# Performance work log

Hardware: AMD Instinct MI355X
Metric: run time of the kernel (lower is better)

The kernel has to match this reference:

```python
import jax, jax.numpy as jnp
from jax import lax
import numpy as np

# ---- config (mirrors cfg_post / cfg_proj) ----
CENTER_THRESHOLD = 0.1
NMS_KERNEL = 7
TOP_K = 128
STUFF_AREA = 2048
LABEL_DIVISOR = 1000
THING_LIST = jnp.array([1, 2, 3, 4, 5, 6, 7], dtype=jnp.int32)
DEPTH_MIN = 0.0
DEPTH_MAX = 6.0
VOXEL_SIZE = 0.0625
TRUNCATION = 3.0
TSDF_THRESH = 1.5  # not Matterport
NUM_CLASSES = 12
B, H, W, G = 2, 256, 256, 96


def setup_inputs() -> dict:
    key = jax.random.key(0)
    ks = jax.random.split(key, 7)
    semantic2d = jax.random.normal(ks[0], (B, NUM_CLASSES, H, W), jnp.float32)
    center2d = jax.random.uniform(ks[1], (B, 1, H, W), jnp.float32)
    offset2d = jax.random.normal(ks[2], (B, 2, H, W), jnp.float32) * 8.0
    geometry = jax.random.normal(ks[3], (B, 1, G, G, G), jnp.float32) * 2.0
    occupancy3d = jax.random.normal(ks[4], (B, 1, G, G, G), jnp.float32)
    semantic3d = jax.random.normal(ks[5], (B, NUM_CLASSES, G, G, G), jnp.float32)
    offset3d = jax.random.normal(ks[6], (B, 3, G, G, G), jnp.float32) * 4.0
    fx = 288.0
    intrinsic = jnp.tile(
        jnp.array([[fx, 0.0, W / 2.0], [0.0, fx, H / 2.0], [0.0, 0.0, 1.0]],
                  jnp.float32)[None], (B, 1, 1))
    return dict(semantic2d=semantic2d, center2d=center2d, offset2d=offset2d,
                geometry=geometry, occupancy3d=occupancy3d,
                semantic3d=semantic3d, offset3d=offset3d, intrinsic=intrinsic)


def _isin_things(x):
    return (x[..., None] == THING_LIST).any(-1)


def _panoptic2d(sem_logits, heat, offset):
    # sem_logits [C,H,W], heat [1,H,W], offset [2,H,W] (dy,dx)
    sem = jnp.argmax(sem_logits, axis=0).astype(jnp.int32)  # [H,W]
    hm = heat[0]
    # heatmap NMS: keep local maxima under a NMS_KERNEL max-pool
    pooled = lax.reduce_window(hm, -jnp.inf, lax.max,
                               (NMS_KERNEL, NMS_KERNEL), (1, 1), 'SAME')
    hm_nms = jnp.where(pooled == hm, hm, 0.0)
    scores, idx = lax.top_k(hm_nms.reshape(-1), TOP_K)
    valid = scores > CENTER_THRESHOLD                       # [K]
    cy = (idx // W).astype(jnp.float32)
    cx = (idx % W).astype(jnp.float32)
    classes = sem[idx // W, idx % W]                        # class at center px
    # per-pixel nearest-center assignment via predicted offsets
    yy, xx = jnp.meshgrid(jnp.arange(H, dtype=jnp.float32),
                          jnp.arange(W, dtype=jnp.float32), indexing='ij')
    py = (yy + offset[0]).reshape(-1, 1)                    # [HW,1]
    px = (xx + offset[1]).reshape(-1, 1)
    d2 = (py - cy[None, :]) ** 2 + (px - cx[None, :]) ** 2  # [HW,K]
    d2 = jnp.where(valid[None, :], d2, jnp.inf)
    inst = jnp.argmin(d2, axis=1).astype(jnp.int32)         # [HW]
    any_valid = valid.any()
    thing_mask = _isin_things(sem)
    # stuff-area filtering
    counts = jax.ops.segment_sum(jnp.ones(H * W, jnp.float32),
                                 sem.reshape(-1), num_segments=NUM_CLASSES)
    stuff_keep = counts[sem] >= STUFF_AREA
    stuff_pan = jnp.where(stuff_keep, sem * LABEL_DIVISOR, 0)
    inst2d = inst.reshape(H, W)
    thing_pan = classes[inst2d] * LABEL_DIVISOR + inst2d + 1
    thing_pan = jnp.where(any_valid, thing_pan, 0)
    pan = jnp.where(thing_mask, thing_pan, stuff_pan)
    return pan, cy, cx, scores, classes, valid


def _panoptic3d(fg, sem3d, offset3d, cy, cx, classes, valid, intr):
    # fg [G,G,G] bool, sem3d [G,G,G] int, offset3d [3,G,G,G]
    fx, fy = intr[0, 0], intr[1, 1]
    u0, v0 = intr[0, 2], intr[1, 2]
    ii, jj, kk = jnp.meshgrid(jnp.arange(G, dtype=jnp.float32),
                              jnp.arange(G, dtype=jnp.float32),
                              jnp.arange(G, dtype=jnp.float32), indexing='ij')
    # shift voxel index by 3D center offset, convert to metric camera coords
    half = G * VOXEL_SIZE / 2.0
    Xm = (ii + offset3d[0] + 0.5) * VOXEL_SIZE - half
    Ym = (jj + offset3d[1] + 0.5) * VOXEL_SIZE - half
    Zm = jnp.clip(DEPTH_MIN + (kk + offset3d[2] + 0.5) * VOXEL_SIZE,
                  0.1, DEPTH_MAX)
    u = (fx * Xm / Zm + u0).reshape(-1, 1)                  # [G^3,1]
    v = (fy * Ym / Zm + v0).reshape(-1, 1)
    d2 = (v - cy[None, :]) ** 2 + (u - cx[None, :]) ** 2    # [G^3,K]
    d2 = jnp.where(valid[None, :], d2, jnp.inf)
    inst = jnp.argmin(d2, axis=1).astype(jnp.int32).reshape(G, G, G)
    any_valid = valid.any()
    thing_mask = _isin_things(sem3d)
    counts = jax.ops.segment_sum(fg.reshape(-1).astype(jnp.float32),
                                 sem3d.reshape(-1), num_segments=NUM_CLASSES)
    stuff_keep = counts[sem3d] >= STUFF_AREA
    stuff_pan = jnp.where(stuff_keep, sem3d * LABEL_DIVISOR, 0)
    thing_pan = classes[inst] * LABEL_DIVISOR + inst + 1
    thing_pan = jnp.where(any_valid, thing_pan, 0)
    pan = jnp.where(thing_mask, thing_pan, stuff_pan)
    return jnp.where(fg, pan, 0)


def reference(semantic2d, center2d, offset2d, geometry, occupancy3d,
              semantic3d, offset3d, intrinsic):
    # pred['geometry'][pred['occupancy3d'] <= 0] = truncation
    geometry = jnp.where(occupancy3d <= 0.0, TRUNCATION, geometry)
    pan2d, cy, cx, scores, classes, valid = jax.vmap(_panoptic2d)(
        semantic2d, center2d, offset2d)
    fg = jnp.abs(geometry[:, 0]) < TSDF_THRESH
    sem3d = jnp.argmax(semantic3d, axis=1).astype(jnp.int32)
    pan3d = jax.vmap(_panoptic3d)(fg, sem3d, offset3d, cy, cx, classes,
                                  valid, intrinsic)
    center_point2d = jnp.stack([cy, cx], axis=-1)  # [B,K,2]
    return pan2d, pan3d, geometry, center_point2d, classes, scores
```

## Files before the change

### kernel.cpp

```cpp
#include <hip/hip_runtime.h>
#include <stdint.h>

constexpr int B = 2, H = 256, W = 256, G = 96, C = 12, K = 128;
constexpr int HW = H * W;
constexpr int G3 = G * G * G;
constexpr float CENTER_THRESHOLD = 0.1f;
constexpr int STUFF_AREA = 2048;
constexpr int LABEL_DIVISOR = 1000;
constexpr float VOXEL_SIZE = 0.0625f;
constexpr float TRUNCATION = 3.0f;
constexpr float TSDF_THRESH = 1.5f;
constexpr float DEPTH_MAX = 6.0f;
constexpr float HALF_EXT = 3.0f;
constexpr int TOPK_CAP = 6144;
constexpr int TOPK_NB = 64;
constexpr int PAN2_BLOCKS = (B * HW) / 1024;
constexpr int F3D_BLOCKS = (B * G3) / 1024;

constexpr size_t O_PAN2 = 0;
constexpr size_t O_PAN3 = 131072;
constexpr size_t O_GEOM = 1900544;
constexpr size_t O_CENT = 3670016;
constexpr size_t O_CLS  = 3670528;
constexpr size_t O_SCR  = 3670784;

constexpr size_t WS_SC   = 2304;
constexpr size_t WS_CL   = 3328;
constexpr size_t WS_SEM2 = 4352;
constexpr size_t WS_NMS  = 135424;
constexpr size_t WS_CV   = 266496;
constexpr size_t WS_CI   = 790784;
constexpr size_t WS_STUF = 1315072;
constexpr size_t WS_CYV  = 3084544;
constexpr size_t WS_CXV  = 3085568;

typedef float f32x2 __attribute__((ext_vector_type(2)));

__device__ inline f32x2 pk_add(f32x2 a, f32x2 b) {
    f32x2 d;
    asm("v_pk_add_f32 %0, %1, %2" : "=v"(d) : "v"(a), "v"(b));
    return d;
}
__device__ inline f32x2 pk_mul(f32x2 a, f32x2 b) {
    f32x2 d;
    asm("v_pk_mul_f32 %0, %1, %2" : "=v"(d) : "v"(a), "v"(b));
    return d;
}

__global__ __launch_bounds__(256)
void k_pre2d(const float* __restrict__ sem2in,
             const float* __restrict__ center2d,
             uint8_t* __restrict__ semMap, uint8_t* __restrict__ nmsMask,
             float* __restrict__ candVal, int* __restrict__ candIdx,
             int* __restrict__ candCount, int* __restrict__ counts2d) {
    __shared__ float vm[2][W];
    __shared__ int lcnt[C];
    int t = threadIdx.x;
    int r = t >> 7;
    int c0 = (t & 127) * 2;
    int b = blockIdx.x / (H / 2);
    int h = (blockIdx.x % (H / 2)) * 2 + r;
    if (t < C) lcnt[t] = 0;
    const float* hmb = center2d + (size_t)b * HW;
    int h0 = max(h - 3, 0), h1 = min(h + 3, H - 1);
    float2 hm2 = *(const float2*)(hmb + h * W + c0);
    float m0 = -INFINITY, m1 = -INFINITY;
    for (int y = h0; y <= h1; ++y) {
        float2 v = *(const float2*)(hmb + y * W + c0);
        m0 = fmaxf(m0, v.x);
        m1 = fmaxf(m1, v.y);
    }
    vm[r][c0] = m0;
    vm[r][c0 + 1] = m1;
    __syncthreads();
    float mm[2];
#pragma unroll
    for (int q = 0; q < 2; ++q) {
        int c = c0 + q;
        int w0 = max(c - 3, 0), w1 = min(c + 3, W - 1);
        float mx = -INFINITY;
        for (int x = w0; x <= w1; ++x) mx = fmaxf(mx, vm[r][x]);
        mm[q] = mx;
    }
    const float* s = sem2in + (size_t)b * C * HW + h * W + c0;
    float2 s0 = *(const float2*)s;
    float bv[2] = {s0.x, s0.y};
    int cls[2] = {0, 0};
#pragma unroll
    for (int c = 1; c < C; ++c) {
        float2 x = *(const float2*)(s + (size_t)c * HW);
        if (x.x > bv[0]) { bv[0] = x.x; cls[0] = c; }
        if (x.y > bv[1]) { bv[1] = x.y; cls[1] = c; }
    }
    int p = h * W + c0;
    int gid = b * HW + p;
    semMap[gid] = (uint8_t)cls[0];
    semMap[gid + 1] = (uint8_t)cls[1];
    atomicAdd(&lcnt[cls[0]], 1);
    atomicAdd(&lcnt[cls[1]], 1);
    float hma[2] = {hm2.x, hm2.y};
#pragma unroll
    for (int q = 0; q < 2; ++q) {
        bool cand = (hma[q] == mm[q]);
        nmsMask[gid + q] = cand ? 1 : 0;
        if (cand) {
            int pos = atomicAdd(&candCount[b], 1);
            if (pos < HW) {
                candVal[(size_t)b * HW + pos] = hma[q];
                candIdx[(size_t)b * HW + pos] = p + q;
            }
        }
    }
    __syncthreads();
    if (t < C) atomicAdd(&counts2d[b * C + t], lcnt[t]);
}

__global__ __launch_bounds__(256)
void k_topk(const uint8_t* __restrict__ semMap, const uint8_t* __restrict__ nmsMask,
            const float* __restrict__ candVal, const int* __restrict__ candIdx,
            const int* __restrict__ candCount,
            float* __restrict__ scA, int* __restrict__ clA,
            float* __restrict__ cyV, float* __restrict__ cxV,
            float* __restrict__ out) {
    __shared__ float2 cd[TOPK_CAP];
    int b = blockIdx.x / TOPK_NB;
    int sub = blockIdx.x % TOPK_NB;
    int t = threadIdx.x;
    int lane = t & 63;
    int wv = sub * 4 + (t >> 6);
    int n = candCount[b];
    if (n > HW) n = HW;
    const float* cv = candVal + (size_t)b * HW;
    const int*  ci = candIdx + (size_t)b * HW;
    bool useLds = (n <= TOPK_CAP);
    if (useLds) {
        for (int i = t; i < n; i += 256)
            cd[i] = make_float2(cv[i], __int_as_float(ci[i]));
    }
    __syncthreads();
    for (int i = wv; i < n; i += TOPK_NB * 4) {
        float v; int id;
        if (useLds) { float2 c = cd[i]; v = c.x; id = __float_as_int(c.y); }
        else        { v = cv[i]; id = ci[i]; }
        int r = 0;
        if (useLds) {
            for (int j = lane; j < n; j += 64) {
                float2 c = cd[j];
                r += (c.x > v) || (c.x == v && __float_as_int(c.y) < id);
            }
        } else {
            for (int j = lane; j < n; j += 64) {
                float vj = cv[j]; int ij = ci[j];
                r += (vj > v) || (vj == v && ij < id);
            }
        }
#pragma unroll
        for (int off = 32; off >= 1; off >>= 1) r += __shfl_xor(r, off, 64);
        if (lane == 0 && r < K) {
            int o = b * K + r;
            float fy = (float)(id / W);
            float fx = (float)(id % W);
            int cls = (int)semMap[(size_t)b * HW + id];
            bool val = v > CENTER_THRESHOLD;
            scA[o] = v; clA[o] = cls;
            cyV[o] = val ? fy : INFINITY;
            cxV[o] = val ? fx : INFINITY;
            out[O_CENT + (size_t)o * 2 + 0] = fy;
            out[O_CENT + (size_t)o * 2 + 1] = fx;
            out[O_CLS + o] = (float)cls;
            out[O_SCR + o] = v;
        }
    }
    if (sub == 0 && t == 0 && n < K) {
        int r = n;
        for (int p = 0; p < HW && r < K; ++p) {
            if (!nmsMask[(size_t)b * HW + p]) {
                int o = b * K + r;
                float fy = (float)(p / W);
                float fx = (float)(p % W);
                int cls = (int)semMap[(size_t)b * HW + p];
                scA[o] = 0.0f; clA[o] = cls;
                cyV[o] = INFINITY;
                cxV[o] = INFINITY;
                out[O_CENT + (size_t)o * 2 + 0] = fy;
                out[O_CENT + (size_t)o * 2 + 1] = fx;
                out[O_CLS + o] = (float)cls;
                out[O_SCR + o] = 0.0f;
                ++r;
            }
        }
    }
}

__device__ inline void argmin128(const float4* __restrict__ cc4,
                                 const float2* __restrict__ cc2,
                                 const f32x2 vv2[2], const f32x2 uu2[2],
                                 int bi[4]) {
#pragma clang fp contract(off)
    f32x2 m0 = {INFINITY, INFINITY}, m1 = {INFINITY, INFINITY};
    int gs[4] = {0, 0, 0, 0};
    for (int g = 0; g < 8; ++g) {
        f32x2 b0 = {INFINITY, INFINITY}, b1 = {INFINITY, INFINITY};
#pragma unroll
        for (int kk = 0; kk < 16; ++kk) {
            float4 c4 = cc4[(g << 4) + kk];
            f32x2 ncy; ncy[0] = c4.x; ncy[1] = c4.y;
            f32x2 ncx; ncx[0] = c4.z; ncx[1] = c4.w;
            f32x2 dv = pk_add(vv2[0], ncy);
            f32x2 du = pk_add(uu2[0], ncx);
            f32x2 d0 = pk_add(pk_mul(dv, dv), pk_mul(du, du));
            dv = pk_add(vv2[1], ncy);
            du = pk_add(uu2[1], ncx);
            f32x2 d1 = pk_add(pk_mul(dv, dv), pk_mul(du, du));
            b0[0] = fminf(b0[0], d0[0]); b0[1] = fminf(b0[1], d0[1]);
            b1[0] = fminf(b1[0], d1[0]); b1[1] = fminf(b1[1], d1[1]);
        }
        if (b0[0] < m0[0]) { m0[0] = b0[0]; gs[0] = g; }
        if (b0[1] < m0[1]) { m0[1] = b0[1]; gs[1] = g; }
        if (b1[0] < m1[0]) { m1[0] = b1[0]; gs[2] = g; }
        if (b1[1] < m1[1]) { m1[1] = b1[1]; gs[3] = g; }
    }
    float vq[4] = {vv2[0][0], vv2[0][1], vv2[1][0], vv2[1][1]};
    float uq[4] = {uu2[0][0], uu2[0][1], uu2[1][0], uu2[1][1]};
    float mq[4] = {m0[0], m0[1], m1[0], m1[1]};
#pragma unroll
    for (int q = 0; q < 4; ++q) {
        int kb = 0;
        int gbase = gs[q] << 4;
#pragma unroll
        for (int kk = 15; kk >= 0; --kk) {
            float2 c2 = cc2[gbase + kk];
            float dv = vq[q] + c2.x;
            float du = uq[q] + c2.y;
            float d = dv * dv + du * du;
            if (d == mq[q]) kb = kk;
        }
        bi[q] = gbase + kb;
    }
}

__global__ __launch_bounds__(256)
void k_fuse(const float* __restrict__ geom, const float* __restrict__ occ,
            const float* __restrict__ sem3in,
            uint8_t* __restrict__ stuffCand, int* __restrict__ counts3d,
            const float* __restrict__ offset2d,
            const uint8_t* __restrict__ semMap,
            const int* __restrict__ counts2d,
            const float* __restrict__ off3,
            const float* __restrict__ intr,
            const float* __restrict__ scA, const int* __restrict__ clA,
            const float* __restrict__ cyV, const float* __restrict__ cxV,
            float* __restrict__ out) {
#pragma clang fp contract(off)
    __shared__ float4 cc4[K];
    __shared__ float2 cc2[K];
    __shared__ int clsL[K];
    __shared__ int lcnt[C];
    __shared__ int cntL[C];
    int t = threadIdx.x;
    if (blockIdx.x < PAN2_BLOCKS) {
        int b = blockIdx.x / (PAN2_BLOCKS / B);
        int base = blockIdx.x * 1024 + t * 4;
        int p = base - b * HW;
        if (t < K) {
            float cy = cyV[b * K + t], cx = cxV[b * K + t];
            cc4[t] = make_float4(-cy, -cy, -cx, -cx);
            cc2[t] = make_float2(-cy, -cx);
            clsL[t] = clA[b * K + t];
        }
        if (t < C) cntL[t] = counts2d[b * C + t];
        __syncthreads();
        bool anyV = scA[b * K] > CENTER_THRESHOLD;
        int h = p / W, w = p % W;
        const float* offb = offset2d + (size_t)b * 2 * HW + p;
        float4 oy = *(const float4*)offb;
        float4 ox = *(const float4*)(offb + HW);
        f32x2 py2[2], px2[2];
        py2[0][0] = (float)h + oy.x;        py2[0][1] = (float)h + oy.y;
        py2[1][0] = (float)h + oy.z;        py2[1][1] = (float)h + oy.w;
        px2[0][0] = (float)(w + 0) + ox.x;  px2[0][1] = (float)(w + 1) + ox.y;
        px2[1][0] = (float)(w + 2) + ox.z;  px2[1][1] = (float)(w + 3) + ox.w;
        int bi[4];
        argmin128(cc4, cc2, py2, px2, bi);
        uchar4 s4 = *(const uchar4*)(semMap + base);
        int sa[4] = {s4.x, s4.y, s4.z, s4.w};
        float pout[4];
#pragma unroll
        for (int q = 0; q < 4; ++q) {
            int sem = sa[q];
            int pan;
            if (sem >= 1 && sem <= 7) {
                pan = anyV ? (clsL[bi[q]] * LABEL_DIVISOR + bi[q] + 1) : 0;
            } else {
                pan = (cntL[sem] >= STUFF_AREA) ? sem * LABEL_DIVISOR : 0;
            }
            pout[q] = (float)pan;
        }
        *(float4*)(out + O_PAN2 + base) = make_float4(pout[0], pout[1], pout[2], pout[3]);
    } else {
        int bid3 = blockIdx.x - PAN2_BLOCKS;
        int b = bid3 / (F3D_BLOCKS / B);
        int base = bid3 * 1024 + t * 4;
        int v = base - b * G3;
        if (t < K) {
            float cy = cyV[b * K + t], cx = cxV[b * K + t];
            cc4[t] = make_float4(-cy, -cy, -cx, -cx);
            cc2[t] = make_float2(-cy, -cx);
            clsL[t] = clA[b * K + t];
        }
        if (t < C) lcnt[t] = 0;
        __syncthreads();
        float4 g = *(const float4*)(geom + base);
        float4 o = *(const float4*)(occ + base);
        float go[4];
        go[0] = (o.x <= 0.0f) ? TRUNCATION : g.x;
        go[1] = (o.y <= 0.0f) ? TRUNCATION : g.y;
        go[2] = (o.z <= 0.0f) ? TRUNCATION : g.z;
        go[3] = (o.w <= 0.0f) ? TRUNCATION : g.w;
        *(float4*)(out + O_GEOM + base) = make_float4(go[0], go[1], go[2], go[3]);
        const float* s = sem3in + (size_t)b * C * G3 + v;
        float4 s0 = *(const float4*)s;
        float bv[4] = {s0.x, s0.y, s0.z, s0.w};
        int bc[4] = {0, 0, 0, 0};
#pragma unroll
        for (int c = 1; c < C; ++c) {
            float4 x = *(const float4*)(s + (size_t)c * G3);
            float xa[4] = {x.x, x.y, x.z, x.w};
#pragma unroll
            for (int q = 0; q < 4; ++q)
                if (xa[q] > bv[q]) { bv[q] = xa[q]; bc[q] = c; }
        }
        bool fg[4];
        uint8_t sc4[4];
#pragma unroll
        for (int q = 0; q < 4; ++q) {
            fg[q] = fabsf(go[q]) < TSDF_THRESH;
            if (fg[q]) atomicAdd(&lcnt[bc[q]], 1);
            sc4[q] = (fg[q] && bc[q] >= 8) ? (uint8_t)bc[q] : 0;
        }
        *(uchar4*)(stuffCand + base) = make_uchar4(sc4[0], sc4[1], sc4[2], sc4[3]);
        float fx = intr[(size_t)b * 9 + 0];
        float fy = intr[(size_t)b * 9 + 4];
        float u0 = intr[(size_t)b * 9 + 2];
        float v0 = intr[(size_t)b * 9 + 5];
        int i = v / (G * G);
        int rem = v - i * (G * G);
        int j = rem / G;
        int k0 = rem - j * G;
        const float* ob = off3 + (size_t)b * 3 * G3 + v;
        float4 o0 = *(const float4*)ob;
        float4 o1 = *(const float4*)(ob + G3);
        float4 o2 = *(const float4*)(ob + 2 * (size_t)G3);
        float oa0[4] = {o0.x, o0.y, o0.z, o0.w};
        float oa1[4] = {o1.x, o1.y, o1.z, o1.w};
        float oa2[4] = {o2.x, o2.y, o2.z, o2.w};
        f32x2 vv2[2], uu2[2];
#pragma unroll
        for (int q = 0; q < 4; ++q) {
            float Xm = ((float)i + oa0[q] + 0.5f) * VOXEL_SIZE - HALF_EXT;
            float Ym = ((float)j + oa1[q] + 0.5f) * VOXEL_SIZE - HALF_EXT;
            float Zr = 0.0f + ((float)(k0 + q) + oa2[q] + 0.5f) * VOXEL_SIZE;
            float Zm = fminf(fmaxf(Zr, 0.1f), DEPTH_MAX);
            uu2[q >> 1][q & 1] = fx * Xm / Zm + u0;
            vv2[q >> 1][q & 1] = fy * Ym / Zm + v0;
        }
        bool anyV = scA[b * K] > CENTER_THRESHOLD;
        int bi[4];
        argmin128(cc4, cc2, vv2, uu2, bi);
        float pout[4];
#pragma unroll
        for (int q = 0; q < 4; ++q) {
            int sem = bc[q];
            int pan = 0;
            if (sem >= 1 && sem <= 7) {
                pan = anyV ? (clsL[bi[q]] * LABEL_DIVISOR + bi[q] + 1) : 0;
                if (!fg[q]) pan = 0;
            }
            pout[q] = (float)pan;
        }
        *(float4*)(out + O_PAN3 + base) = make_float4(pout[0], pout[1], pout[2], pout[3]);
        __syncthreads();
        if (t < C) atomicAdd(&counts3d[b * C + t], lcnt[t]);
    }
}

__global__ __launch_bounds__(256)
void k_stuff(const uint8_t* __restrict__ stuffCand,
             const int* __restrict__ counts3d,
             float* __restrict__ out) {
    __shared__ int cntL[C];
    constexpr int BPB = F3D_BLOCKS / 4 / B;
    int t = threadIdx.x;
    int b = blockIdx.x / BPB;
    if (t < C) cntL[t] = counts3d[b * C + t];
    __syncthreads();
    int base = blockIdx.x * 4096 + t * 16;
    uint4 packed = *(const uint4*)(stuffCand + base);
    uint32_t wds[4] = {packed.x, packed.y, packed.z, packed.w};
#pragma unroll
    for (int wq = 0; wq < 4; ++wq) {
        uint32_t wd = wds[wq];
#pragma unroll
        for (int bq = 0; bq < 4; ++bq) {
            int c = (wd >> (8 * bq)) & 0xFF;
            if (c != 0 && cntL[c] >= STUFF_AREA) {
                out[O_PAN3 + base + wq * 4 + bq] = (float)(c * LABEL_DIVISOR);
            }
        }
    }
}

extern "C" void kernel_launch(void* const* d_in, const int* in_sizes, int n_in,
                              void* d_out, int out_size, void* d_ws, size_t ws_size,
                              hipStream_t stream) {
    const float* semantic2d  = (const float*)d_in[0];
    const float* center2d    = (const float*)d_in[1];
    const float* offset2d    = (const float*)d_in[2];
    const float* geometry    = (const float*)d_in[3];
    const float* occupancy3d = (const float*)d_in[4];
    const float* semantic3d  = (const float*)d_in[5];
    const float* offset3d    = (const float*)d_in[6];
    const float* intrinsic   = (const float*)d_in[7];
    float* out = (float*)d_out;
    char* ws = (char*)d_ws;

    int* candCount = (int*)(ws + 0);
    int* counts2d  = (int*)(ws + 16);
    int* counts3d  = (int*)(ws + 112);
    float* scA = (float*)(ws + WS_SC);
    int*   clA = (int*)(ws + WS_CL);
    uint8_t* semMap  = (uint8_t*)(ws + WS_SEM2);
    uint8_t* nmsMask = (uint8_t*)(ws + WS_NMS);
    float* candVal = (float*)(ws + WS_CV);
    int*   candIdx = (int*)(ws + WS_CI);
    uint8_t* stuffCand = (uint8_t*)(ws + WS_STUF);
    float* cyV = (float*)(ws + WS_CYV);
    float* cxV = (float*)(ws + WS_CXV);

    hipMemsetAsync(d_ws, 0, 256, stream);

    k_pre2d<<<B * (H / 2), 256, 0, stream>>>(semantic2d, center2d, semMap, nmsMask,
                                             candVal, candIdx, candCount, counts2d);
    k_topk<<<B * TOPK_NB, 256, 0, stream>>>(semMap, nmsMask, candVal, candIdx, candCount,
                                            scA, clA, cyV, cxV, out);
    k_fuse<<<PAN2_BLOCKS + F3D_BLOCKS, 256, 0, stream>>>(
        geometry, occupancy3d, semantic3d, stuffCand, counts3d,
        offset2d, semMap, counts2d, offset3d, intrinsic,
        scA, clA, cyV, cxV, out);
    k_stuff<<<F3D_BLOCKS / 4, 256, 0, stream>>>(stuffCand, counts3d, out);
}
```

Before: 93.66 us.

## Widen pre2d to four pixels per thread, count only stuff classes, cap fuse registers

k_pre2d now handles four pixels per thread with float4 loads and uchar4 stores, so half as many blocks are launched. Both k_pre2d and k_fuse now count only classes 8 and above, which cuts shared atomics, presumably because only those counts feed the stuff-area test. k_fuse gets launch_bounds(256,8), partial unrolling of its argmin and class loops, and packed class and foreground bits, all aimed at fewer registers and higher occupancy. The risks are spills or lost ILP from the register cap, and the counts for classes 0-7 are never filled, which breaks any consumer that still reads them.

```diff
diff --git a/kernel.cpp b/kernel.cpp
--- a/kernel.cpp
+++ b/kernel.cpp
@@ -53,29 +53,28 @@
              uint8_t* __restrict__ semMap, uint8_t* __restrict__ nmsMask,
              float* __restrict__ candVal, int* __restrict__ candIdx,
              int* __restrict__ candCount, int* __restrict__ counts2d) {
-    __shared__ float vm[2][W];
-    __shared__ int lcnt[C];
+    __shared__ float vm[4][W];
+    __shared__ int lcnt[4];
     int t = threadIdx.x;
-    int r = t >> 7;
-    int c0 = (t & 127) * 2;
-    int b = blockIdx.x / (H / 2);
-    int h = (blockIdx.x % (H / 2)) * 2 + r;
-    if (t < C) lcnt[t] = 0;
+    int r = t >> 6;
+    int c0 = (t & 63) * 4;
+    int b = blockIdx.x / (H / 4);
+    int h = (blockIdx.x % (H / 4)) * 4 + r;
+    if (t < 4) lcnt[t] = 0;
     const float* hmb = center2d + (size_t)b * HW;
     int h0 = max(h - 3, 0), h1 = min(h + 3, H - 1);
-    float2 hm2 = *(const float2*)(hmb + h * W + c0);
-    float m0 = -INFINITY, m1 = -INFINITY;
+    float4 hm4 = *(const float4*)(hmb + h * W + c0);
+    float m0 = -INFINITY, m1 = -INFINITY, m2 = -INFINITY, m3 = -INFINITY;
     for (int y = h0; y <= h1; ++y) {
-        float2 v = *(const float2*)(hmb + y * W + c0);
-        m0 = fmaxf(m0, v.x);
-        m1 = fmaxf(m1, v.y);
-    }
-    vm[r][c0] = m0;
-    vm[r][c0 + 1] = m1;
+        float4 v = *(const float4*)(hmb + y * W + c0);
+        m0 = fmaxf(m0, v.x); m1 = fmaxf(m1, v.y);
+        m2 = fmaxf(m2, v.z); m3 = fmaxf(m3, v.w);
+    }
+    *(float4*)&vm[r][c0] = make_float4(m0, m1, m2, m3);
     __syncthreads();
-    float mm[2];
-#pragma unroll
-    for (int q = 0; q < 2; ++q) {
+    float mm[4];
+#pragma unroll
+    for (int q = 0; q < 4; ++q) {
         int c = c0 + q;
         int w0 = max(c - 3, 0), w1 = min(c + 3, W - 1);
         float mx = -INFINITY;
@@ -83,24 +82,25 @@
         mm[q] = mx;
     }
     const float* s = sem2in + (size_t)b * C * HW + h * W + c0;
-    float2 s0 = *(const float2*)s;
-    float bv[2] = {s0.x, s0.y};
-    int cls[2] = {0, 0};
-#pragma unroll
+    float4 s0 = *(const float4*)s;
+    float bv[4] = {s0.x, s0.y, s0.z, s0.w};
+    int cls[4] = {0, 0, 0, 0};
+#pragma unroll 4
     for (int c = 1; c < C; ++c) {
-        float2 x = *(const float2*)(s + (size_t)c * HW);
-        if (x.x > bv[0]) { bv[0] = x.x; cls[0] = c; }
-        if (x.y > bv[1]) { bv[1] = x.y; cls[1] = c; }
+        float4 x = *(const float4*)(s + (size_t)c * HW);
+        float xa[4] = {x.x, x.y, x.z, x.w};
+#pragma unroll
+        for (int q = 0; q < 4; ++q)
+            if (xa[q] > bv[q]) { bv[q] = xa[q]; cls[q] = c; }
     }
     int p = h * W + c0;
     int gid = b * HW + p;
-    semMap[gid] = (uint8_t)cls[0];
-    semMap[gid + 1] = (uint8_t)cls[1];
-    atomicAdd(&lcnt[cls[0]], 1);
-    atomicAdd(&lcnt[cls[1]], 1);
-    float hma[2] = {hm2.x, hm2.y};
-#pragma unroll
-    for (int q = 0; q < 2; ++q) {
+    *(uchar4*)(semMap + gid) =
+        make_uchar4((uint8_t)cls[0], (uint8_t)cls[1], (uint8_t)cls[2], (uint8_t)cls[3]);
+    float hma[4] = {hm4.x, hm4.y, hm4.z, hm4.w};
+#pragma unroll
+    for (int q = 0; q < 4; ++q) {
+        if (cls[q] >= 8) atomicAdd(&lcnt[cls[q] - 8], 1);
         bool cand = (hma[q] == mm[q]);
         nmsMask[gid + q] = cand ? 1 : 0;
         if (cand) {
@@ -112,7 +112,7 @@
         }
     }
     __syncthreads();
-    if (t < C) atomicAdd(&counts2d[b * C + t], lcnt[t]);
+    if (t < 4) atomicAdd(&counts2d[b * C + 8 + t], lcnt[t]);
 }
 
 __global__ __launch_bounds__(256)
@@ -192,16 +192,16 @@
     }
 }
 
-__device__ inline void argmin128(const float4* __restrict__ cc4,
-                                 const float2* __restrict__ cc2,
-                                 const f32x2 vv2[2], const f32x2 uu2[2],
-                                 int bi[4]) {
+__device__ __forceinline__ void argmin128(const float4* __restrict__ cc4,
+                                          const float2* __restrict__ cc2,
+                                          const f32x2 vv2[2], const f32x2 uu2[2],
+                                          int bi[4]) {
 #pragma clang fp contract(off)
     f32x2 m0 = {INFINITY, INFINITY}, m1 = {INFINITY, INFINITY};
     int gs[4] = {0, 0, 0, 0};
     for (int g = 0; g < 8; ++g) {
         f32x2 b0 = {INFINITY, INFINITY}, b1 = {INFINITY, INFINITY};
-#pragma unroll
+#pragma unroll 4
         for (int kk = 0; kk < 16; ++kk) {
             float4 c4 = cc4[(g << 4) + kk];
             f32x2 ncy; ncy[0] = c4.x; ncy[1] = c4.y;
@@ -227,7 +227,7 @@
     for (int q = 0; q < 4; ++q) {
         int kb = 0;
         int gbase = gs[q] << 4;
-#pragma unroll
+#pragma unroll 8
         for (int kk = 15; kk >= 0; --kk) {
             float2 c2 = cc2[gbase + kk];
             float dv = vq[q] + c2.x;
@@ -239,7 +239,7 @@
     }
 }
 
-__global__ __launch_bounds__(256)
+__global__ __launch_bounds__(256, 8)
 void k_fuse(const float* __restrict__ geom, const float* __restrict__ occ,
             const float* __restrict__ sem3in,
             uint8_t* __restrict__ stuffCand, int* __restrict__ counts3d,
@@ -255,7 +255,7 @@
     __shared__ float4 cc4[K];
     __shared__ float2 cc2[K];
     __shared__ int clsL[K];
-    __shared__ int lcnt[C];
+    __shared__ int lcnt[4];
     __shared__ int cntL[C];
     int t = threadIdx.x;
     if (blockIdx.x < PAN2_BLOCKS) {
@@ -308,7 +308,7 @@
             cc2[t] = make_float2(-cy, -cx);
             clsL[t] = clA[b * K + t];
         }
-        if (t < C) lcnt[t] = 0;
+        if (t < 4) lcnt[t] = 0;
         __syncthreads();
         float4 g = *(const float4*)(geom + base);
         float4 o = *(const float4*)(occ + base);
@@ -322,7 +322,7 @@
         float4 s0 = *(const float4*)s;
         float bv[4] = {s0.x, s0.y, s0.z, s0.w};
         int bc[4] = {0, 0, 0, 0};
-#pragma unroll
+#pragma unroll 4
         for (int c = 1; c < C; ++c) {
             float4 x = *(const float4*)(s + (size_t)c * G3);
             float xa[4] = {x.x, x.y, x.z, x.w};
@@ -330,13 +330,15 @@
             for (int q = 0; q < 4; ++q)
                 if (xa[q] > bv[q]) { bv[q] = xa[q]; bc[q] = c; }
         }
-        bool fg[4];
+        int bcp = 0, fgm = 0;
         uint8_t sc4[4];
 #pragma unroll
         for (int q = 0; q < 4; ++q) {
-            fg[q] = fabsf(go[q]) < TSDF_THRESH;
-            if (fg[q]) atomicAdd(&lcnt[bc[q]], 1);
-            sc4[q] = (fg[q] && bc[q] >= 8) ? (uint8_t)bc[q] : 0;
+            bool fgq = fabsf(go[q]) < TSDF_THRESH;
+            sc4[q] = (fgq && bc[q] >= 8) ? (uint8_t)bc[q] : 0;
+            if (sc4[q]) atomicAdd(&lcnt[bc[q] - 8], 1);
+            bcp |= bc[q] << (8 * q);
+            fgm |= (fgq ? 1 : 0) << q;
         }
         *(uchar4*)(stuffCand + base) = make_uchar4(sc4[0], sc4[1], sc4[2], sc4[3]);
         float fx = intr[(size_t)b * 9 + 0];
@@ -370,17 +372,17 @@
         float pout[4];
 #pragma unroll
         for (int q = 0; q < 4; ++q) {
-            int sem = bc[q];
+            int sem = (bcp >> (8 * q)) & 0xFF;
             int pan = 0;
             if (sem >= 1 && sem <= 7) {
                 pan = anyV ? (clsL[bi[q]] * LABEL_DIVISOR + bi[q] + 1) : 0;
-                if (!fg[q]) pan = 0;
+                if (!((fgm >> q) & 1)) pan = 0;
             }
             pout[q] = (float)pan;
         }
         *(float4*)(out + O_PAN3 + base) = make_float4(pout[0], pout[1], pout[2], pout[3]);
         __syncthreads();
-        if (t < C) atomicAdd(&counts3d[b * C + t], lcnt[t]);
+        if (t < 4) atomicAdd(&counts3d[b * C + 8 + t], lcnt[t]);
     }
 }
 
@@ -439,7 +441,7 @@
 
     hipMemsetAsync(d_ws, 0, 256, stream);
 
-    k_pre2d<<<B * (H / 2), 256, 0, stream>>>(semantic2d, center2d, semMap, nmsMask,
+    k_pre2d<<<B * (H / 4), 256, 0, stream>>>(semantic2d, center2d, semMap, nmsMask,
                                              candVal, candIdx, candCount, counts2d);
     k_topk<<<B * TOPK_NB, 256, 0, stream>>>(semMap, nmsMask, candVal, candIdx, candCount,
                                             scA, clA, cyV, cxV, out);
```

Measured after the change: 162.9 us. 1.74x slower.
